# Optimization experiments

Measured on AMD Instinct MI355X. Metric: run time of the kernel, lower is better.

Reference implementation:

```python
import jax, jax.numpy as jnp
import numpy as np

B, S, D = 16, 2048, 1024  # batch, max_len, inp_size == hidden_size


def setup_inputs() -> dict:
    key = jax.random.key(0)
    k1, k2, k3, k4, k5, k6 = jax.random.split(key, 6)
    stdv = 1.0 / np.sqrt(D)
    return {
        "encoder_outputs": jax.random.normal(k1, (B, S, D), dtype=jnp.float32),
        "hidden": jax.random.normal(k2, (B, D), dtype=jnp.float32),
        "lengths": jax.random.randint(k3, (B,), 1, S + 1, dtype=jnp.int32),
        "W": jax.random.normal(k4, (D, 2 * D), dtype=jnp.float32) * stdv,
        "b": jax.random.normal(k5, (D,), dtype=jnp.float32) * stdv,
        "v": jax.random.normal(k6, (D,), dtype=jnp.float32) * stdv,
    }


def reference(encoder_outputs, hidden, lengths, W, b, v):
    # Linear on cat([H, enc]) == H @ Wh^T + enc @ We^T + b (avoids materializing the concat)
    Wh, We = W[:, :D], W[:, D:]              # [D_out, D] each
    hid_proj = hidden @ Wh.T                  # [B, D]
    enc_proj = jnp.einsum('bsd,ed->bse', encoder_outputs, We)  # [B, S, D]
    energy = jnp.tanh(enc_proj + hid_proj[:, None, :] + b)     # [B, S, D]
    scores = jnp.einsum('bsd,d->bs', energy, v)                # [B, S]
    # mask positions >= length to -inf before softmax
    valid = jnp.arange(S)[None, :] < lengths[:, None]          # [B, S]
    scores = jnp.where(valid, scores, -jnp.inf)
    attn = jax.nn.softmax(scores, axis=-1)                     # [B, S]
    context = jnp.einsum('bs,bsd->bd', attn, encoder_outputs)  # [B, D]
    return context[:, None, :]                                 # [B, 1, D] to match torch bmm output
```

## Files before the change

### kernel.cpp

```cpp
#include <hip/hip_runtime.h>
#include <cstdint>

#define DEV static __device__ __forceinline__

typedef __attribute__((__ext_vector_type__(8))) __bf16 bf16x8;
typedef __attribute__((__ext_vector_type__(4))) float f32x4;

static constexpr int Bc = 16, Sc = 2048, Dc = 1024;

DEV unsigned short f2bf(float x) {
  unsigned int u = __float_as_uint(x);
  unsigned int r = (u + 0x7fffu + ((u >> 16) & 1u)) >> 16;
  return (unsigned short)r;
}
DEV unsigned int pack2(float a, float b) {
  return (unsigned int)f2bf(a) | ((unsigned int)f2bf(b) << 16);
}
DEV float tanh_fast(float x) {
  return 1.f - 2.f / (__expf(2.f * x) + 1.f);
}
DEV void gload16(const void* g, void* l) {
  __builtin_amdgcn_global_load_lds(
      (const __attribute__((address_space(1))) unsigned int*)g,
      (__attribute__((address_space(3))) unsigned int*)l, 16, 0, 0);
}

__global__ __launch_bounds__(256) void k_cvt_enc(const float* __restrict__ in,
                                                 unsigned short* __restrict__ out,
                                                 const int* __restrict__ lengths) {
  int team = threadIdx.x >> 7;
  int lane = threadIdx.x & 127;
  int r0 = blockIdx.x * 16;
  int b = r0 >> 11;
  int len = lengths[b];
  for (int rr = team; rr < 16; rr += 2) {
    int s = (r0 + rr) & 2047;
    if (s >= len) continue;
    const float* src = in + (size_t)(r0 + rr) * Dc + lane * 8;
    unsigned short* dst = out + (size_t)(r0 + rr) * Dc + lane * 8;
    float4 f0 = *(const float4*)src;
    float4 f1 = *(const float4*)(src + 4);
    uint4 o;
    o.x = pack2(f0.x, f0.y);
    o.y = pack2(f0.z, f0.w);
    o.z = pack2(f1.x, f1.y);
    o.w = pack2(f1.z, f1.w);
    *(uint4*)dst = o;
  }
}

__global__ __launch_bounds__(256) void k_cvt_We(const float* __restrict__ W,
                                                unsigned short* __restrict__ out) {
  int i = (blockIdx.x * 256 + threadIdx.x) * 8;
  int e = i >> 10, d = i & 1023;
  const float* p = W + (size_t)e * 2048 + 1024 + d;
  float4 f0 = *(const float4*)p;
  float4 f1 = *(const float4*)(p + 4);
  uint4 o;
  o.x = pack2(f0.x, f0.y);
  o.y = pack2(f0.z, f0.w);
  o.z = pack2(f1.x, f1.y);
  o.w = pack2(f1.z, f1.w);
  *(uint4*)(out + i) = o;
}

__global__ __launch_bounds__(256) void k_hidproj(const float* __restrict__ hidden,
                                                 const float* __restrict__ W,
                                                 const float* __restrict__ bias,
                                                 float* __restrict__ hp) {
  __shared__ float wrow[Dc];
  int e = blockIdx.x, t = threadIdx.x;
  for (int i = t; i < Dc; i += 256) wrow[i] = W[(size_t)e * 2048 + i];
  __syncthreads();
  int w = t >> 6, lane = t & 63;
  float bv = bias[e];
  for (int bi = w; bi < Bc; bi += 4) {
    float s = 0.f;
    const float* hrow = hidden + (size_t)bi * Dc;
    for (int d = lane; d < Dc; d += 64) s += hrow[d] * wrow[d];
    for (int m = 1; m < 64; m <<= 1) s += __shfl_xor(s, m);
    if (lane == 0) hp[(size_t)bi * Dc + e] = s + bv;
  }
}

__global__ __launch_bounds__(256) void k_worklist(const int* __restrict__ lengths,
                                                  int* __restrict__ wl) {
  int t = threadIdx.x;
  int sblk = t >> 4, b = t & 15;
  int active = (sblk * 128 < lengths[b]) ? 1 : 0;
  unsigned long long mask = __ballot(active);
  int lane = t & 63, wid = t >> 6;
  int prefix = __popcll(mask & ((1ull << lane) - 1ull));
  __shared__ int woff[4];
  if (lane == 0) woff[wid] = __popcll(mask);
  __syncthreads();
  int base = 0;
  for (int i = 0; i < wid; i++) base += woff[i];
  if (active) wl[1 + base + prefix] = (b << 8) | sblk;
  if (t == 0) wl[0] = woff[0] + woff[1] + woff[2] + woff[3];
}

__global__ __launch_bounds__(256) void k_scores(const unsigned short* __restrict__ Ae,
                                                const unsigned short* __restrict__ We,
                                                const float* __restrict__ hp,
                                                const float* __restrict__ v,
                                                const int* __restrict__ wl,
                                                float* __restrict__ pscores) {
  int g = blockIdx.x & 255;
  int et = blockIdx.x >> 8;
  if (g >= wl[0]) return;
  int pk = wl[1 + g];
  int b = pk >> 8, sblk = pk & 255;
  int s0 = sblk * 128;
  int m0 = b * Sc + s0;
  int e0 = et * 128;

  __shared__ unsigned short As0[128 * 32];
  __shared__ unsigned short As1[128 * 32];
  __shared__ unsigned short Bs0[128 * 32];
  __shared__ unsigned short Bs1[128 * 32];
  __shared__ float hp_s[128], v_s[128], sc_s[128];

  int t = threadIdx.x;
  int w = t >> 6, lane = t & 63;
  if (t < 128) {
    hp_s[t] = hp[(size_t)b * Dc + e0 + t];
    v_s[t] = v[e0 + t];
    sc_s[t] = 0.f;
  }
  asm volatile("s_waitcnt vmcnt(0)" ::: "memory");

  f32x4 acc[4][4] = {};
  int wr = w >> 1, wc = w & 1;
  const unsigned short* ga0 = Ae + (size_t)(m0 + (t >> 2)) * Dc + (t & 3) * 8;
  const unsigned short* gb0 = We + (size_t)(e0 + (t >> 2)) * Dc + (t & 3) * 8;

  int kc = (lane >> 4) * 8;
  int ar = (wr * 64 + (lane & 15)) * 32 + kc;
  int br = (wc * 64 + (lane & 15)) * 32 + kc;

  auto stage = [&](int k0, unsigned short* A, unsigned short* B) {
    gload16(ga0 + k0, A + w * 512);
    gload16(ga0 + k0 + 64 * Dc, A + 2048 + w * 512);
    gload16(gb0 + k0, B + w * 512);
    gload16(gb0 + k0 + 64 * Dc, B + 2048 + w * 512);
  };
  auto compute = [&](const unsigned short* A, const unsigned short* B) {
    bf16x8 af[4], bfr[4];
#pragma unroll
    for (int m = 0; m < 4; m++)
      af[m] = __builtin_bit_cast(bf16x8, *(const uint4*)(A + ar + m * 512));
#pragma unroll
    for (int n = 0; n < 4; n++)
      bfr[n] = __builtin_bit_cast(bf16x8, *(const uint4*)(B + br + n * 512));
#pragma unroll
    for (int m = 0; m < 4; m++)
#pragma unroll
      for (int n = 0; n < 4; n++)
        acc[m][n] = __builtin_amdgcn_mfma_f32_16x16x32_bf16(af[m], bfr[n], acc[m][n], 0, 0, 0);
  };

  stage(0, As0, Bs0);

#pragma unroll 1
  for (int i2 = 0; i2 < 15; ++i2) {
    stage((2 * i2 + 1) * 32, As1, Bs1);
    asm volatile("s_waitcnt vmcnt(4)" ::: "memory");
    __builtin_amdgcn_sched_barrier(0);
    __builtin_amdgcn_s_barrier();
    __builtin_amdgcn_sched_barrier(0);
    compute(As0, Bs0);
    __builtin_amdgcn_sched_barrier(0);
    __builtin_amdgcn_s_barrier();
    stage((2 * i2 + 2) * 32, As0, Bs0);
    asm volatile("s_waitcnt vmcnt(4)" ::: "memory");
    __builtin_amdgcn_sched_barrier(0);
    __builtin_amdgcn_s_barrier();
    __builtin_amdgcn_sched_barrier(0);
    compute(As1, Bs1);
    __builtin_amdgcn_sched_barrier(0);
    __builtin_amdgcn_s_barrier();
  }
  stage(31 * 32, As1, Bs1);
  asm volatile("s_waitcnt vmcnt(4)" ::: "memory");
  __builtin_amdgcn_sched_barrier(0);
  __builtin_amdgcn_s_barrier();
  __builtin_amdgcn_sched_barrier(0);
  compute(As0, Bs0);
  __builtin_amdgcn_sched_barrier(0);
  __builtin_amdgcn_s_barrier();
  asm volatile("s_waitcnt vmcnt(0)" ::: "memory");
  __builtin_amdgcn_sched_barrier(0);
  __builtin_amdgcn_s_barrier();
  __builtin_amdgcn_sched_barrier(0);
  compute(As1, Bs1);

  for (int m = 0; m < 4; m++) {
    float rs0 = 0.f, rs1 = 0.f, rs2 = 0.f, rs3 = 0.f;
    for (int n = 0; n < 4; n++) {
      int ec = wc * 64 + n * 16 + (lane & 15);
      float hpv = hp_s[ec], vv = v_s[ec];
      f32x4 a = acc[m][n];
      rs0 += vv * tanh_fast(a[0] + hpv);
      rs1 += vv * tanh_fast(a[1] + hpv);
      rs2 += vv * tanh_fast(a[2] + hpv);
      rs3 += vv * tanh_fast(a[3] + hpv);
    }
    for (int mask = 1; mask < 16; mask <<= 1) {
      rs0 += __shfl_xor(rs0, mask);
      rs1 += __shfl_xor(rs1, mask);
      rs2 += __shfl_xor(rs2, mask);
      rs3 += __shfl_xor(rs3, mask);
    }
    if ((lane & 15) == 0) {
      int rbase = wr * 64 + m * 16 + (lane >> 4) * 4;
      atomicAdd(&sc_s[rbase + 0], rs0);
      atomicAdd(&sc_s[rbase + 1], rs1);
      atomicAdd(&sc_s[rbase + 2], rs2);
      atomicAdd(&sc_s[rbase + 3], rs3);
    }
  }
  __syncthreads();
  if (t < 128) pscores[((size_t)et * Bc + b) * Sc + s0 + t] = sc_s[t];
}

__global__ __launch_bounds__(256) void k_softmax(const float* __restrict__ pscores,
                                                 const int* __restrict__ lengths,
                                                 float* __restrict__ attn) {
  int b = blockIdx.x, t = threadIdx.x;
  int len = lengths[b];
  float vals[8];
  float mx = -INFINITY;
  for (int i = 0; i < 8; i++) {
    int s = t + i * 256;
    float sc = 0.f;
    for (int p = 0; p < 8; p++) sc += pscores[((size_t)p * Bc + b) * Sc + s];
    sc = (s < len) ? sc : -INFINITY;
    vals[i] = sc;
    mx = fmaxf(mx, sc);
  }
  for (int m = 1; m < 64; m <<= 1) mx = fmaxf(mx, __shfl_xor(mx, m));
  __shared__ float rmax[4], rsum[4];
  int w = t >> 6, lane = t & 63;
  if (lane == 0) rmax[w] = mx;
  __syncthreads();
  mx = fmaxf(fmaxf(rmax[0], rmax[1]), fmaxf(rmax[2], rmax[3]));
  float sm = 0.f;
  for (int i = 0; i < 8; i++) {
    vals[i] = __expf(vals[i] - mx);
    sm += vals[i];
  }
  for (int m = 1; m < 64; m <<= 1) sm += __shfl_xor(sm, m);
  if (lane == 0) rsum[w] = sm;
  __syncthreads();
  sm = rsum[0] + rsum[1] + rsum[2] + rsum[3];
  float inv = 1.f / sm;
  for (int i = 0; i < 8; i++) attn[(size_t)b * Sc + t + i * 256] = vals[i] * inv;
}

__global__ __launch_bounds__(256) void k_ctx(const unsigned short* __restrict__ ebf,
                                             const float* __restrict__ attn,
                                             const int* __restrict__ lengths,
                                             float* __restrict__ pctx) {
  int b = blockIdx.x >> 4, sp = blockIdx.x & 15;
  int t = threadIdx.x;
  int d0 = t * 4;
  int sbeg = sp * 128;
  float* outp = pctx + ((size_t)sp * Bc + b) * Dc + d0;
  int len = lengths[b];
  if (sbeg >= len) {
    *(float4*)outp = make_float4(0.f, 0.f, 0.f, 0.f);
    return;
  }
  __shared__ float at_s[128];
  if (t < 128) at_s[t] = attn[(size_t)b * Sc + sbeg + t];
  __syncthreads();
  float4 a = make_float4(0.f, 0.f, 0.f, 0.f);
  const unsigned short* ebase = ebf + ((size_t)b * Sc + sbeg) * Dc + d0;
  int ns = min(128, len - sbeg);
  for (int i = 0; i < ns; i++) {
    float wt = at_s[i];
    uint2 u = *(const uint2*)(ebase + (size_t)i * Dc);
    a.x += wt * __uint_as_float(u.x << 16);
    a.y += wt * __uint_as_float(u.x & 0xffff0000u);
    a.z += wt * __uint_as_float(u.y << 16);
    a.w += wt * __uint_as_float(u.y & 0xffff0000u);
  }
  *(float4*)outp = a;
}

__global__ __launch_bounds__(256) void k_reduce(const float* __restrict__ pctx,
                                               float* __restrict__ out) {
  int i = blockIdx.x * 256 + threadIdx.x;
  int b = i >> 10, d = i & 1023;
  float s = 0.f;
  for (int p = 0; p < 16; p++) s += pctx[((size_t)p * Bc + b) * Dc + d];
  out[i] = s;
}

extern "C" void kernel_launch(void* const* d_in, const int* in_sizes, int n_in,
                              void* d_out, int out_size, void* d_ws, size_t ws_size,
                              hipStream_t stream) {
  const float* enc = (const float*)d_in[0];
  const float* hidden = (const float*)d_in[1];
  const int* lengths = (const int*)d_in[2];
  const float* W = (const float*)d_in[3];
  const float* bias = (const float*)d_in[4];
  const float* v = (const float*)d_in[5];
  float* out = (float*)d_out;

  char* ws = (char*)d_ws;
  unsigned short* ebf = (unsigned short*)ws;
  unsigned short* webf = (unsigned short*)(ws + 67108864);
  float* hp = (float*)(ws + 69206016);
  float* pscores = (float*)(ws + 69271552);
  float* attn = (float*)(ws + 70320128);
  float* pctx = (float*)(ws + 70451200);
  int* wl = (int*)(ws + 70516736);

  hipLaunchKernelGGL(k_cvt_enc, dim3(2048), dim3(256), 0, stream, enc, ebf, lengths);
  hipLaunchKernelGGL(k_cvt_We, dim3(512), dim3(256), 0, stream, W, webf);
  hipLaunchKernelGGL(k_hidproj, dim3(1024), dim3(256), 0, stream, hidden, W, bias, hp);
  hipLaunchKernelGGL(k_worklist, dim3(1), dim3(256), 0, stream, lengths, wl);
  hipLaunchKernelGGL(k_scores, dim3(2048), dim3(256), 0, stream, ebf, webf, hp, v,
                     wl, pscores);
  hipLaunchKernelGGL(k_softmax, dim3(16), dim3(256), 0, stream, pscores, lengths, attn);
  hipLaunchKernelGGL(k_ctx, dim3(256), dim3(256), 0, stream, ebf, attn, lengths, pctx);
  hipLaunchKernelGGL(k_reduce, dim3(64), dim3(256), 0, stream, pctx, out);
}
```

Baseline: 111.3 us.

## Fuse encoder bf16 conversion into scores GEMM and merge worklist into hidproj

Drops the separate pass that converts encoder outputs to bf16. The scores GEMM now loads fp32 encoder tiles into registers, packs them with v_cvt_pk_bf16_f32 and writes them to LDS. The context kernel reads fp32 encoder data directly, and the worklist build moves into block 0 of the hidden-projection kernel, which removes a launch. The bf16 copy's write and re-read traffic goes away. In exchange, the GEMM reads twice as many A bytes per tile from L2/HBM, and the pipeline now drains all outstanding loads each step (vmcnt(0)), which can expose memory latency.

Measured after the change: 111.7 us. No clear change (+0.3%).

```diff
diff --git a/kernel.cpp b/kernel.cpp
--- a/kernel.cpp
+++ b/kernel.cpp
@@ -16,6 +16,11 @@
 DEV unsigned int pack2(float a, float b) {
   return (unsigned int)f2bf(a) | ((unsigned int)f2bf(b) << 16);
 }
+DEV unsigned int cvtpk(float lo, float hi) {
+  unsigned int r;
+  asm("v_cvt_pk_bf16_f32 %0, %1, %2" : "=v"(r) : "v"(lo), "v"(hi));
+  return r;
+}
 DEV float tanh_fast(float x) {
   return 1.f - 2.f / (__expf(2.f * x) + 1.f);
 }
@@ -23,30 +28,6 @@
   __builtin_amdgcn_global_load_lds(
       (const __attribute__((address_space(1))) unsigned int*)g,
       (__attribute__((address_space(3))) unsigned int*)l, 16, 0, 0);
-}
-
-__global__ __launch_bounds__(256) void k_cvt_enc(const float* __restrict__ in,
-                                                 unsigned short* __restrict__ out,
-                                                 const int* __restrict__ lengths) {
-  int team = threadIdx.x >> 7;
-  int lane = threadIdx.x & 127;
-  int r0 = blockIdx.x * 16;
-  int b = r0 >> 11;
-  int len = lengths[b];
-  for (int rr = team; rr < 16; rr += 2) {
-    int s = (r0 + rr) & 2047;
-    if (s >= len) continue;
-    const float* src = in + (size_t)(r0 + rr) * Dc + lane * 8;
-    unsigned short* dst = out + (size_t)(r0 + rr) * Dc + lane * 8;
-    float4 f0 = *(const float4*)src;
-    float4 f1 = *(const float4*)(src + 4);
-    uint4 o;
-    o.x = pack2(f0.x, f0.y);
-    o.y = pack2(f0.z, f0.w);
-    o.z = pack2(f1.x, f1.y);
-    o.w = pack2(f1.z, f1.w);
-    *(uint4*)dst = o;
-  }
 }
 
 __global__ __launch_bounds__(256) void k_cvt_We(const float* __restrict__ W,
@@ -67,9 +48,26 @@
 __global__ __launch_bounds__(256) void k_hidproj(const float* __restrict__ hidden,
                                                  const float* __restrict__ W,
                                                  const float* __restrict__ bias,
-                                                 float* __restrict__ hp) {
+                                                 float* __restrict__ hp,
+                                                 const int* __restrict__ lengths,
+                                                 int* __restrict__ wl) {
+  int t = threadIdx.x;
+  if (blockIdx.x == 0) {
+    int sblk = t >> 4, b = t & 15;
+    int active = (sblk * 128 < lengths[b]) ? 1 : 0;
+    unsigned long long mask = __ballot(active);
+    int lane = t & 63, wid = t >> 6;
+    int prefix = __popcll(mask & ((1ull << lane) - 1ull));
+    __shared__ int woff[4];
+    if (lane == 0) woff[wid] = __popcll(mask);
+    __syncthreads();
+    int base = 0;
+    for (int i = 0; i < wid; i++) base += woff[i];
+    if (active) wl[1 + base + prefix] = (b << 8) | sblk;
+    if (t == 0) wl[0] = woff[0] + woff[1] + woff[2] + woff[3];
+  }
   __shared__ float wrow[Dc];
-  int e = blockIdx.x, t = threadIdx.x;
+  int e = blockIdx.x;
   for (int i = t; i < Dc; i += 256) wrow[i] = W[(size_t)e * 2048 + i];
   __syncthreads();
   int w = t >> 6, lane = t & 63;
@@ -83,24 +81,7 @@
   }
 }
 
-__global__ __launch_bounds__(256) void k_worklist(const int* __restrict__ lengths,
-                                                  int* __restrict__ wl) {
-  int t = threadIdx.x;
-  int sblk = t >> 4, b = t & 15;
-  int active = (sblk * 128 < lengths[b]) ? 1 : 0;
-  unsigned long long mask = __ballot(active);
-  int lane = t & 63, wid = t >> 6;
-  int prefix = __popcll(mask & ((1ull << lane) - 1ull));
-  __shared__ int woff[4];
-  if (lane == 0) woff[wid] = __popcll(mask);
-  __syncthreads();
-  int base = 0;
-  for (int i = 0; i < wid; i++) base += woff[i];
-  if (active) wl[1 + base + prefix] = (b << 8) | sblk;
-  if (t == 0) wl[0] = woff[0] + woff[1] + woff[2] + woff[3];
-}
-
-__global__ __launch_bounds__(256) void k_scores(const unsigned short* __restrict__ Ae,
+__global__ __launch_bounds__(256) void k_scores(const float* __restrict__ enc,
                                                 const unsigned short* __restrict__ We,
                                                 const float* __restrict__ hp,
                                                 const float* __restrict__ v,
@@ -128,22 +109,35 @@
     v_s[t] = v[e0 + t];
     sc_s[t] = 0.f;
   }
-  asm volatile("s_waitcnt vmcnt(0)" ::: "memory");
 
   f32x4 acc[4][4] = {};
   int wr = w >> 1, wc = w & 1;
-  const unsigned short* ga0 = Ae + (size_t)(m0 + (t >> 2)) * Dc + (t & 3) * 8;
+  const float* gaF = enc + (size_t)(m0 + (t >> 2)) * Dc + (t & 3) * 8;
   const unsigned short* gb0 = We + (size_t)(e0 + (t >> 2)) * Dc + (t & 3) * 8;
 
   int kc = (lane >> 4) * 8;
   int ar = (wr * 64 + (lane & 15)) * 32 + kc;
   int br = (wc * 64 + (lane & 15)) * 32 + kc;
 
-  auto stage = [&](int k0, unsigned short* A, unsigned short* B) {
-    gload16(ga0 + k0, A + w * 512);
-    gload16(ga0 + k0 + 64 * Dc, A + 2048 + w * 512);
+  float4 a0, a1, a2, a3;
+  auto ldA = [&](int k0) {
+    a0 = *(const float4*)(gaF + k0);
+    a1 = *(const float4*)(gaF + k0 + 4);
+    a2 = *(const float4*)(gaF + k0 + 64 * Dc);
+    a3 = *(const float4*)(gaF + k0 + 64 * Dc + 4);
+  };
+  auto gldB = [&](int k0, unsigned short* B) {
     gload16(gb0 + k0, B + w * 512);
     gload16(gb0 + k0 + 64 * Dc, B + 2048 + w * 512);
+  };
+  auto writeA = [&](unsigned short* A) {
+    uint4 w0, w1;
+    w0.x = cvtpk(a0.x, a0.y); w0.y = cvtpk(a0.z, a0.w);
+    w0.z = cvtpk(a1.x, a1.y); w0.w = cvtpk(a1.z, a1.w);
+    w1.x = cvtpk(a2.x, a2.y); w1.y = cvtpk(a2.z, a2.w);
+    w1.z = cvtpk(a3.x, a3.y); w1.w = cvtpk(a3.z, a3.w);
+    *(uint4*)(A + t * 8) = w0;
+    *(uint4*)(A + 2048 + t * 8) = w1;
   };
   auto compute = [&](const unsigned short* A, const unsigned short* B) {
     bf16x8 af[4], bfr[4];
@@ -159,40 +153,40 @@
       for (int n = 0; n < 4; n++)
         acc[m][n] = __builtin_amdgcn_mfma_f32_16x16x32_bf16(af[m], bfr[n], acc[m][n], 0, 0, 0);
   };
-
-  stage(0, As0, Bs0);
-
-#pragma unroll 1
-  for (int i2 = 0; i2 < 15; ++i2) {
-    stage((2 * i2 + 1) * 32, As1, Bs1);
-    asm volatile("s_waitcnt vmcnt(4)" ::: "memory");
+  auto drain_barrier = [&]() {
+    asm volatile("s_waitcnt vmcnt(0) lgkmcnt(0)" ::: "memory");
     __builtin_amdgcn_sched_barrier(0);
     __builtin_amdgcn_s_barrier();
     __builtin_amdgcn_sched_barrier(0);
+  };
+
+  ldA(0);
+  gldB(0, Bs0);
+  writeA(As0);
+  __syncthreads();
+
+#pragma unroll 1
+  for (int i2 = 0; i2 < 15; ++i2) {
+    int k1 = (2 * i2 + 1) * 32, k2 = (2 * i2 + 2) * 32;
+    ldA(k1);
+    gldB(k1, Bs1);
+    __builtin_amdgcn_sched_barrier(0);
     compute(As0, Bs0);
-    __builtin_amdgcn_sched_barrier(0);
-    __builtin_amdgcn_s_barrier();
-    stage((2 * i2 + 2) * 32, As0, Bs0);
-    asm volatile("s_waitcnt vmcnt(4)" ::: "memory");
-    __builtin_amdgcn_sched_barrier(0);
-    __builtin_amdgcn_s_barrier();
+    writeA(As1);
+    drain_barrier();
+    ldA(k2);
+    gldB(k2, Bs0);
     __builtin_amdgcn_sched_barrier(0);
     compute(As1, Bs1);
-    __builtin_amdgcn_sched_barrier(0);
-    __builtin_amdgcn_s_barrier();
-  }
-  stage(31 * 32, As1, Bs1);
-  asm volatile("s_waitcnt vmcnt(4)" ::: "memory");
-  __builtin_amdgcn_sched_barrier(0);
-  __builtin_amdgcn_s_barrier();
+    writeA(As0);
+    drain_barrier();
+  }
+  ldA(31 * 32);
+  gldB(31 * 32, Bs1);
   __builtin_amdgcn_sched_barrier(0);
   compute(As0, Bs0);
-  __builtin_amdgcn_sched_barrier(0);
-  __builtin_amdgcn_s_barrier();
-  asm volatile("s_waitcnt vmcnt(0)" ::: "memory");
-  __builtin_amdgcn_sched_barrier(0);
-  __builtin_amdgcn_s_barrier();
-  __builtin_amdgcn_sched_barrier(0);
+  writeA(As1);
+  drain_barrier();
   compute(As1, Bs1);
 
   for (int m = 0; m < 4; m++) {
@@ -258,7 +252,7 @@
   for (int i = 0; i < 8; i++) attn[(size_t)b * Sc + t + i * 256] = vals[i] * inv;
 }
 
-__global__ __launch_bounds__(256) void k_ctx(const unsigned short* __restrict__ ebf,
+__global__ __launch_bounds__(256) void k_ctx(const float* __restrict__ enc,
                                              const float* __restrict__ attn,
                                              const int* __restrict__ lengths,
                                              float* __restrict__ pctx) {
@@ -276,15 +270,15 @@
   if (t < 128) at_s[t] = attn[(size_t)b * Sc + sbeg + t];
   __syncthreads();
   float4 a = make_float4(0.f, 0.f, 0.f, 0.f);
-  const unsigned short* ebase = ebf + ((size_t)b * Sc + sbeg) * Dc + d0;
+  const float* ebase = enc + ((size_t)b * Sc + sbeg) * Dc + d0;
   int ns = min(128, len - sbeg);
   for (int i = 0; i < ns; i++) {
     float wt = at_s[i];
-    uint2 u = *(const uint2*)(ebase + (size_t)i * Dc);
-    a.x += wt * __uint_as_float(u.x << 16);
-    a.y += wt * __uint_as_float(u.x & 0xffff0000u);
-    a.z += wt * __uint_as_float(u.y << 16);
-    a.w += wt * __uint_as_float(u.y & 0xffff0000u);
+    float4 e = *(const float4*)(ebase + (size_t)i * Dc);
+    a.x += wt * e.x;
+    a.y += wt * e.y;
+    a.z += wt * e.z;
+    a.w += wt * e.w;
   }
   *(float4*)outp = a;
 }
@@ -310,21 +304,19 @@
   float* out = (float*)d_out;
 
   char* ws = (char*)d_ws;
-  unsigned short* ebf = (unsigned short*)ws;
-  unsigned short* webf = (unsigned short*)(ws + 67108864);
-  float* hp = (float*)(ws + 69206016);
-  float* pscores = (float*)(ws + 69271552);
-  float* attn = (float*)(ws + 70320128);
-  float* pctx = (float*)(ws + 70451200);
-  int* wl = (int*)(ws + 70516736);
-
-  hipLaunchKernelGGL(k_cvt_enc, dim3(2048), dim3(256), 0, stream, enc, ebf, lengths);
+  unsigned short* webf = (unsigned short*)ws;
+  float* hp = (float*)(ws + 2097152);
+  float* pscores = (float*)(ws + 2161664);
+  float* attn = (float*)(ws + 3210240);
+  float* pctx = (float*)(ws + 3338240);
+  int* wl = (int*)(ws + 4386816);
+
   hipLaunchKernelGGL(k_cvt_We, dim3(512), dim3(256), 0, stream, W, webf);
-  hipLaunchKernelGGL(k_hidproj, dim3(1024), dim3(256), 0, stream, hidden, W, bias, hp);
-  hipLaunchKernelGGL(k_worklist, dim3(1), dim3(256), 0, stream, lengths, wl);
-  hipLaunchKernelGGL(k_scores, dim3(2048), dim3(256), 0, stream, ebf, webf, hp, v,
+  hipLaunchKernelGGL(k_hidproj, dim3(1024), dim3(256), 0, stream, hidden, W, bias, hp,
+                     lengths, wl);
+  hipLaunchKernelGGL(k_scores, dim3(2048), dim3(256), 0, stream, enc, webf, hp, v,
                      wl, pscores);
   hipLaunchKernelGGL(k_softmax, dim3(16), dim3(256), 0, stream, pscores, lengths, attn);
-  hipLaunchKernelGGL(k_ctx, dim3(256), dim3(256), 0, stream, ebf, attn, lengths, pctx);
+  hipLaunchKernelGGL(k_ctx, dim3(256), dim3(256), 0, stream, enc, attn, lengths, pctx);
   hipLaunchKernelGGL(k_reduce, dim3(64), dim3(256), 0, stream, pctx, out);
 }
```
